# Kernel tuning notes

Hardware: AMD Instinct MI355X
Metric: run time of the kernel (lower is better)

The kernel has to match this reference:

```python
import jax, jax.numpy as jnp
import numpy as np

BS, N, D_N, D_PROJ, ROLE_DIM, K, F, H, L = 4, 1024, 128, 64, 16, 512, 512, 8, 4
HD = F // H
FF = 4 * F
EB_HID = max(H, 8)
TOK_IN = 3 + 3 * D_PROJ + ROLE_DIM + 2  # 213


def _ln(x, g, b, eps=1e-5):
    m = x.mean(-1, keepdims=True)
    v = ((x - m) ** 2).mean(-1, keepdims=True)
    return (x - m) * jax.lax.rsqrt(v + eps) * g + b


def _gelu(x):
    return jax.nn.gelu(x, approximate=False)  # torch nn.GELU default is exact erf


def setup_inputs():
    key = jax.random.key(0)
    ks = jax.random.split(key, 32)
    p = lambda i, shape, s=0.02: jax.random.normal(ks[i], shape, jnp.float32) * s
    return {
        'h': jax.random.normal(ks[0], (BS, N, D_N), jnp.float32),
        'msg': jax.random.normal(ks[1], (BS, N, D_N), jnp.float32),
        'received': jax.random.normal(ks[2], (BS, N, D_N), jnp.float32),
        'W': jax.random.normal(ks[3], (BS, N, N), jnp.float32) * 0.1,
        'hebbian': jax.random.normal(ks[4], (BS, N, N), jnp.float32) * 0.1,
        'decay': jax.random.uniform(ks[5], (BS, N), jnp.float32),
        's_live': jax.random.normal(ks[6], (BS,), jnp.float32),
        's_ema': jax.random.normal(ks[7], (BS,), jnp.float32),
        'role_id': jax.random.randint(ks[8], (N,), 0, 3),
        'Wh': p(9, (D_N, D_PROJ)),
        'Wme': p(10, (D_N, D_PROJ)),
        'Wmr': p(11, (D_N, D_PROJ)),
        'role_emb': p(12, (3, ROLE_DIM)),
        'tok_W1': p(13, (TOK_IN, F)), 'tok_b1': jnp.zeros((F,), jnp.float32),
        'tok_W2': p(14, (F, F)), 'tok_b2': jnp.zeros((F,), jnp.float32),
        'eb_W1': p(15, (3, EB_HID)), 'eb_b1': jnp.zeros((EB_HID,), jnp.float32),
        'eb_W2': p(16, (EB_HID, H)), 'eb_b2': jnp.zeros((H,), jnp.float32),
        'ln1_g': jnp.ones((L, F), jnp.float32), 'ln1_b': jnp.zeros((L, F), jnp.float32),
        'qkv_W': p(17, (L, F, 3 * F)),
        'out_W': p(18, (L, F, F)),
        'ln2_g': jnp.ones((L, F), jnp.float32), 'ln2_b': jnp.zeros((L, F), jnp.float32),
        'ffn_W1': p(19, (L, F, FF)), 'ffn_b1': jnp.zeros((L, FF), jnp.float32),
        'ffn_W2': p(20, (L, FF, F)), 'ffn_b2': jnp.zeros((L, F), jnp.float32),
        'pool_g': jnp.ones((F,), jnp.float32), 'pool_b': jnp.zeros((F,), jnp.float32),
        'head_W': p(21, (F, K)), 'head_b': jnp.zeros((K,), jnp.float32),
    }


def _forward(h, msg, received, W, hebbian, decay, s_live, s_ema, role_id,
             Wh, Wme, Wmr, role_emb, tok_W1, tok_b1, tok_W2, tok_b2,
             eb_W1, eb_b1, eb_W2, eb_b2, ln1_g, ln1_b, qkv_W, out_W,
             ln2_g, ln2_b, ffn_W1, ffn_b1, ffn_W2, ffn_b2,
             pool_g, pool_b, head_W, head_b):
    # ---- build_tokens: [BS,N,F] ----
    h_p = h @ Wh
    me_p = msg @ Wme
    mr_p = received @ Wmr
    h_norm = jnp.linalg.norm(h, axis=-1, keepdims=True)
    msg_norm = jnp.linalg.norm(msg, axis=-1, keepdims=True)
    dec = decay[..., None]
    role_e = jnp.broadcast_to(role_emb[role_id][None], (BS, N, ROLE_DIM))
    sl = jnp.broadcast_to(s_live[:, None, None], (BS, N, 1))
    se = jnp.broadcast_to(s_ema[:, None, None], (BS, N, 1))
    tok_in = jnp.concatenate([h_norm, msg_norm, dec, h_p, me_p, mr_p, role_e, sl, se], axis=-1)
    tokens = _gelu(tok_in @ tok_W1 + tok_b1) @ tok_W2 + tok_b2
    # ---- build_edge_bias: [BS,H,N,N] ----
    asym = W - jnp.swapaxes(W, -1, -2)
    ef = jnp.stack([W, hebbian, asym], axis=-1)           # [BS,N,N,3]
    bias = _gelu(ef @ eb_W1 + eb_b1) @ eb_W2 + eb_b2      # [BS,N,N,H]
    bias = jnp.transpose(bias, (0, 3, 1, 2))              # [BS,H,N,N]
    # ---- attention blocks ----
    scale = 1.0 / np.sqrt(HD).astype(np.float32)
    x = tokens
    for l in range(L):
        hn = _ln(x, ln1_g[l], ln1_b[l])
        qkv = (hn @ qkv_W[l]).reshape(BS, N, 3, H, HD)
        q = jnp.transpose(qkv[:, :, 0], (0, 2, 1, 3))     # [BS,H,N,HD]
        k = jnp.transpose(qkv[:, :, 1], (0, 2, 1, 3))
        v = jnp.transpose(qkv[:, :, 2], (0, 2, 1, 3))
        scores = jnp.einsum('bhnd,bhmd->bhnm', q, k) * scale + bias
        attn = jax.nn.softmax(scores, axis=-1)
        ao = jnp.einsum('bhnm,bhmd->bhnd', attn, v)
        ao = jnp.transpose(ao, (0, 2, 1, 3)).reshape(BS, N, F)
        x = x + ao @ out_W[l]
        hn2 = _ln(x, ln2_g[l], ln2_b[l])
        x = x + _gelu(hn2 @ ffn_W1[l] + ffn_b1[l]) @ ffn_W2[l] + ffn_b2[l]
    pooled = _ln(x, pool_g, pool_b).mean(axis=1)
    logits = pooled @ head_W + head_b
    return logits, x


def reference(h, msg, received, W, hebbian, decay, s_live, s_ema, role_id,
              Wh, Wme, Wmr, role_emb, tok_W1, tok_b1, tok_W2, tok_b2,
              eb_W1, eb_b1, eb_W2, eb_b2, ln1_g, ln1_b, qkv_W, out_W,
              ln2_g, ln2_b, ffn_W1, ffn_b1, ffn_W2, ffn_b2,
              pool_g, pool_b, head_W, head_b):
    return _forward(h, msg, received, W, hebbian, decay, s_live, s_ema, role_id,
                    Wh, Wme, Wmr, role_emb, tok_W1, tok_b1, tok_W2, tok_b2,
                    eb_W1, eb_b1, eb_W2, eb_b2, ln1_g, ln1_b, qkv_W, out_W,
                    ln2_g, ln2_b, ffn_W1, ffn_b1, ffn_W2, ffn_b2,
                    pool_g, pool_b, head_W, head_b)
```

## Files before the change

kernel.cpp:

```cpp
#include <hip/hip_runtime.h>
#include <hip/hip_bf16.h>
#include <math.h>

#define BS 4
#define N_ 1024
#define DN 128
#define DP 64
#define RD 16
#define KOUT 512
#define F_ 512
#define H_ 8
#define HD_ 64
#define L_ 4
#define FFN_ 2048
#define TI 213
#define TIP 256

typedef __attribute__((ext_vector_type(8))) short bf16x8;
typedef __attribute__((ext_vector_type(4))) float f32x4;
typedef unsigned int u32;
typedef unsigned short u16;

union U8 { u32 w[4]; bf16x8 v; };

__device__ __forceinline__ float gelu_fast(float x) {
    float u2 = 1.5957691216f * fmaf(0.044715f * x, x * x, x);
    return x / (1.f + __expf(-u2));
}

__device__ __forceinline__ float gelu_small(float u) {
    float q = u * u;
    float t = fmaf(q, -0.06649038f, 0.39894228f);
    return fmaf(q, t, 0.5f * u);
}

__device__ __forceinline__ void gl_lds16(const void* g, void* l) {
    __builtin_amdgcn_global_load_lds((const __attribute__((address_space(1))) void*)g,
                                     (__attribute__((address_space(3))) void*)l, 16, 0, 0);
}

__device__ __forceinline__ u32 bf16rn(float f) {
    u32 b = __builtin_bit_cast(u32, f);
    return (b + 0x7fffu + ((b >> 16) & 1u)) >> 16;
}
__device__ __forceinline__ float bf2f(u16 u) {
    return __builtin_bit_cast(float, (u32)u << 16);
}

__global__ __launch_bounds__(256) void k_tokin(
    const float* __restrict__ h, const float* __restrict__ msg, const float* __restrict__ rcv,
    const float* __restrict__ decay, const float* __restrict__ s_live, const float* __restrict__ s_ema,
    const int* __restrict__ role_id, const float* __restrict__ role_emb,
    const float* __restrict__ Wh, const float* __restrict__ Wme, const float* __restrict__ Wmr,
    __hip_bfloat16* __restrict__ tok_in)
{
    int row = blockIdx.x;
    int b = row >> 10, n = row & 1023;
    __shared__ float hs[DN], ms[DN], rs[DN];
    __shared__ float proj[192];
    __shared__ float norms[2];
    int tid = threadIdx.x;
    const float* hp = h + (size_t)row * DN;
    const float* mp = msg + (size_t)row * DN;
    const float* rp = rcv + (size_t)row * DN;
    for (int i = tid; i < DN; i += 256) { hs[i] = hp[i]; ms[i] = mp[i]; rs[i] = rp[i]; }
    __syncthreads();
    if (tid < 128) {
        int lane = tid & 63;
        const float* src = (tid < 64) ? hs : ms;
        float v = src[lane]*src[lane] + src[lane+64]*src[lane+64];
        #pragma unroll
        for (int m = 32; m >= 1; m >>= 1) v += __shfl_xor(v, m);
        if (lane == 0) norms[tid >> 6] = sqrtf(v);
    }
    if (tid < 192) {
        int which = tid >> 6, col = tid & 63;
        const float* src = (which == 0) ? hs : ((which == 1) ? ms : rs);
        const float* Wp  = (which == 0) ? Wh : ((which == 1) ? Wme : Wmr);
        float acc = 0.f;
        for (int k2 = 0; k2 < DN; ++k2) acc = fmaf(src[k2], Wp[k2 * DP + col], acc);
        proj[tid] = acc;
    }
    __syncthreads();
    __hip_bfloat16* out = tok_in + (size_t)row * TIP;
    if (tid < TIP) {
        float v = 0.f;
        if (tid == 0) v = norms[0];
        else if (tid == 1) v = norms[1];
        else if (tid == 2) v = decay[b * N_ + n];
        else if (tid < 195) v = proj[tid - 3];
        else if (tid < 211) v = role_emb[role_id[n] * RD + (tid - 195)];
        else if (tid == 211) v = s_live[b];
        else if (tid == 212) v = s_ema[b];
        out[tid] = __float2bfloat16(v);
    }
}

__global__ __launch_bounds__(256) void k_convall(
    const float* __restrict__ qkvW, const float* __restrict__ outW,
    const float* __restrict__ f1W, const float* __restrict__ f2W,
    const float* __restrict__ t1, const float* __restrict__ t2,
    __hip_bfloat16* __restrict__ wq, __hip_bfloat16* __restrict__ wo,
    __hip_bfloat16* __restrict__ w1, __hip_bfloat16* __restrict__ w2,
    __hip_bfloat16* __restrict__ t1w, __hip_bfloat16* __restrict__ t2w)
{
    int tile = blockIdx.x;
    const float* in; __hip_bfloat16* out;
    int K, N, Kpad, r2, nx, ky;
    if (tile < 3072) {
        int z = tile / 768; r2 = tile % 768;
        nx = r2 % 48; ky = r2 / 48;
        in = qkvW + (size_t)z * F_ * 3 * F_; out = wq + (size_t)z * 3 * F_ * F_;
        K = F_; N = 3 * F_; Kpad = F_;
    } else if (tile < 4096) {
        int t = tile - 3072; int z = t / 256; r2 = t % 256;
        nx = r2 % 16; ky = r2 / 16;
        in = outW + (size_t)z * F_ * F_; out = wo + (size_t)z * F_ * F_;
        K = F_; N = F_; Kpad = F_;
    } else if (tile < 8192) {
        int t = tile - 4096; int z = t / 1024; r2 = t % 1024;
        nx = r2 % 64; ky = r2 / 64;
        in = f1W + (size_t)z * F_ * FFN_; out = w1 + (size_t)z * FFN_ * F_;
        K = F_; N = FFN_; Kpad = F_;
    } else if (tile < 12288) {
        int t = tile - 8192; int z = t / 1024; r2 = t % 1024;
        nx = r2 % 16; ky = r2 / 16;
        in = f2W + (size_t)z * FFN_ * F_; out = w2 + (size_t)z * F_ * FFN_;
        K = FFN_; N = F_; Kpad = FFN_;
    } else if (tile < 12416) {
        int t = tile - 12288;
        nx = t % 16; ky = t / 16;
        in = t1; out = t1w; K = TI; N = F_; Kpad = TIP;
    } else {
        int t = tile - 12416;
        nx = t % 16; ky = t / 16;
        in = t2; out = t2w; K = F_; N = F_; Kpad = F_;
    }
    int k0 = ky * 32, n0 = nx * 32;
    __shared__ float tls[32][33];
    int c = threadIdx.x & 31, r = threadIdx.x >> 5;
    #pragma unroll
    for (int i = 0; i < 4; ++i) {
        int rr = r + i*8;
        tls[rr][c] = (k0 + rr < K) ? in[(size_t)(k0 + rr) * N + n0 + c] : 0.f;
    }
    __syncthreads();
    #pragma unroll
    for (int i = 0; i < 4; ++i) {
        int rr = r + i*8;
        out[(size_t)(n0 + rr) * Kpad + k0 + c] = __float2bfloat16(tls[c][rr]);
    }
}

template<int BM, int BN, int EPI, bool OBF>
__global__ __launch_bounds__(256) void k_gemm_bf16(
    const __hip_bfloat16* __restrict__ Ah, int lda,
    const __hip_bfloat16* __restrict__ Bth, int ldb,
    void* __restrict__ Cout, int ldc, int Kc,
    const float* __restrict__ bias,
    const float* __restrict__ resid, int ldres,
    void* __restrict__ aux)
{
    constexpr int MFM = BM / 32;
    constexpr int MFN = BN / 32;
    constexpr int HALF = (BM + BN) * 64;
    constexpr int NLOAD = (BM + BN) / 32;
    constexpr int ACH = BM / 32;
    __shared__ __align__(16) short lds[2 * HALF];
    const short* A  = (const short*)Ah;
    const short* Bt = (const short*)Bth;
    int tid = threadIdx.x, w = tid >> 6, lane = tid & 63;
    int wr = w >> 1, wc = w & 1;
    int m0 = blockIdx.y * BM, n0 = blockIdx.x * BN;

    f32x4 acc[MFM][MFN];
    #pragma unroll
    for (int m = 0; m < MFM; ++m)
        #pragma unroll
        for (int n = 0; n < MFN; ++n)
            acc[m][n] = (f32x4){0.f, 0.f, 0.f, 0.f};

    int ebase = w * 512 + lane * 8;

    auto stage = [&](int buf, int k0) {
        short* L = lds + buf * HALF;
        #pragma unroll
        for (int i = 0; i < NLOAD; ++i) {
            int e = i * 2048 + ebase;
            if (i < ACH) {
                int r = e >> 6, c = e & 63;
                int cs = c ^ (8 * (r & 7));
                gl_lds16(A + (size_t)(m0 + r) * lda + k0 + cs, L + e);
            } else {
                int eb = e - BM * 64;
                int r = eb >> 6, c = eb & 63;
                int cs = c ^ (8 * (r & 7));
                gl_lds16(Bt + (size_t)(n0 + r) * ldb + k0 + cs, L + e);
            }
        }
    };

    int nt = Kc >> 6;
    int buf = 0;
    stage(0, 0);
    __syncthreads();
    int cl = lane & 15, g = lane >> 4;
    for (int t = 0; t < nt; ++t) {
        if (t + 1 < nt) stage(buf ^ 1, (t + 1) << 6);
        const short* La = lds + buf * HALF;
        const short* Lb = La + BM * 64;
        #pragma unroll
        for (int kk = 0; kk < 2; ++kk) {
            bf16x8 av[MFM], bv[MFN];
            #pragma unroll
            for (int m = 0; m < MFM; ++m) {
                int r = wr * (BM/2) + m * 16 + cl;
                av[m] = *(const bf16x8*)&La[r * 64 + ((kk*32 + g*8) ^ (8*(r&7)))];
            }
            #pragma unroll
            for (int n = 0; n < MFN; ++n) {
                int r = wc * (BN/2) + n * 16 + cl;
                bv[n] = *(const bf16x8*)&Lb[r * 64 + ((kk*32 + g*8) ^ (8*(r&7)))];
            }
            #pragma unroll
            for (int m = 0; m < MFM; ++m)
                #pragma unroll
                for (int n = 0; n < MFN; ++n)
                    acc[m][n] = __builtin_amdgcn_mfma_f32_16x16x32_bf16(av[m], bv[n], acc[m][n], 0, 0, 0);
        }
        __syncthreads();
        buf ^= 1;
    }

    int r4 = g * 4;

    if (EPI == 5) {
        __hip_bfloat16* Cb = (__hip_bfloat16*)Cout;
        u16* vtp = (u16*)aux;
        if (n0 >= 1024) {
            int bb = m0 >> 10;
            #pragma unroll
            for (int m = 0; m < MFM; ++m) {
                int grow0 = m0 + wr * (BM/2) + m * 16 + r4;
                int nloc = grow0 & 1023;
                #pragma unroll
                for (int n = 0; n < MFN; ++n) {
                    int rel = n0 - 1024 + wc * (BN / 2) + n * 16 + cl;
                    int hh2 = rel >> 6, d = rel & 63;
                    u32 lo = bf16rn(acc[m][n][0]) | (bf16rn(acc[m][n][1]) << 16);
                    u32 hi = bf16rn(acc[m][n][2]) | (bf16rn(acc[m][n][3]) << 16);
                    uint2 v2 = {lo, hi};
                    *(uint2*)&vtp[((size_t)((bb * 8 + hh2) * 64 + d)) * 1024 + nloc] = v2;
                }
            }
        } else {
            #pragma unroll
            for (int m = 0; m < MFM; ++m) {
                #pragma unroll
                for (int n = 0; n < MFN; ++n) {
                    int gcol = n0 + wc * (BN / 2) + n * 16 + cl;
                    #pragma unroll
                    for (int r = 0; r < 4; ++r) {
                        int grow = m0 + wr * (BM/2) + m * 16 + r4 + r;
                        Cb[(size_t)grow * ldc + gcol] = __float2bfloat16(acc[m][n][r]);
                    }
                }
            }
        }
        return;
    }

    float* Cf = (float*)Cout;
    __hip_bfloat16* Cb = (__hip_bfloat16*)Cout;
    #pragma unroll
    for (int m = 0; m < MFM; ++m) {
        #pragma unroll
        for (int n = 0; n < MFN; ++n) {
            int gcol = n0 + wc * (BN / 2) + n * 16 + cl;
            #pragma unroll
            for (int r = 0; r < 4; ++r) {
                int grow = m0 + wr * (BM/2) + m * 16 + r4 + r;
                float v = acc[m][n][r];
                if (EPI == 1 || EPI == 2 || EPI == 3) v += bias[gcol];
                if (EPI == 2) v = gelu_fast(v);
                if (EPI == 3 || EPI == 4) v += resid[(size_t)grow * ldres + gcol];
                if (OBF) Cb[(size_t)grow * ldc + gcol] = __float2bfloat16(v);
                else     Cf[(size_t)grow * ldc + gcol] = v;
            }
        }
    }
}

__global__ __launch_bounds__(256) void k_ln(const float* __restrict__ x, const float* __restrict__ g,
                                            const float* __restrict__ bb, __hip_bfloat16* __restrict__ out)
{
    int w = threadIdx.x >> 6, lane = threadIdx.x & 63;
    int row = blockIdx.x * 4 + w;
    const float* xr = x + (size_t)row * F_;
    float v[8];
    float s = 0.f;
    #pragma unroll
    for (int i = 0; i < 8; ++i) { v[i] = xr[lane + 64*i]; s += v[i]; }
    #pragma unroll
    for (int m = 32; m >= 1; m >>= 1) s += __shfl_xor(s, m);
    float mean = s * (1.f/512.f);
    float vs = 0.f;
    #pragma unroll
    for (int i = 0; i < 8; ++i) { float d = v[i] - mean; vs = fmaf(d, d, vs); }
    #pragma unroll
    for (int m = 32; m >= 1; m >>= 1) vs += __shfl_xor(vs, m);
    float rstd = rsqrtf(vs * (1.f/512.f) + 1e-5f);
    __hip_bfloat16* orow = out + (size_t)row * F_;
    #pragma unroll
    for (int i = 0; i < 8; ++i) {
        int c = lane + 64*i;
        orow[c] = __float2bfloat16((v[i] - mean) * rstd * g[c] + bb[c]);
    }
}

__global__ __launch_bounds__(256) void k_bias(
    const float* __restrict__ W, const float* __restrict__ Heb,
    const float* __restrict__ eW1, const float* __restrict__ eb1,
    const float* __restrict__ eW2, const float* __restrict__ eb2,
    u16* __restrict__ bias_out)
{
    int b = blockIdx.z;
    int i0 = blockIdx.x * 128, j0 = blockIdx.y * 32;
    __shared__ float Wt[128][33];
    __shared__ float Ht[128][33];
    __shared__ float Wr[32][128];
    const float* Wb = W + (size_t)b * N_ * N_;
    const float* Hb = Heb + (size_t)b * N_ * N_;
    int tid = threadIdx.x;
    {
        int c2 = tid & 31, r = tid >> 5;
        #pragma unroll
        for (int k = 0; k < 16; ++k) {
            int rr = r + k * 8;
            Wt[rr][c2] = Wb[(size_t)(i0 + rr) * N_ + j0 + c2];
            Ht[rr][c2] = Hb[(size_t)(i0 + rr) * N_ + j0 + c2];
        }
        int r2 = tid >> 3, c8 = (tid & 7) * 16;
        #pragma unroll
        for (int k = 0; k < 4; ++k)
            *(float4*)&Wr[r2][c8 + 4*k] = *(const float4*)&Wb[(size_t)(j0 + r2) * N_ + i0 + c8 + 4*k];
    }
    float A[8], Bc[8], Cc[8], Dd[8], W2[8][8], b2v[8];
    #pragma unroll
    for (int k = 0; k < 8; ++k) {
        A[k] = eW1[k]; Bc[k] = eW1[8 + k]; Cc[k] = eW1[16 + k]; Dd[k] = eb1[k];
        b2v[k] = eb2[k];
        #pragma unroll
        for (int hh = 0; hh < 8; ++hh) W2[k][hh] = eW2[k * 8 + hh];
    }
    __syncthreads();
    int c = tid & 31;
    int j8 = tid >> 5;
    #pragma unroll
    for (int pass = 0; pass < 4; ++pass) {
        int jj = j8 + pass * 8;
        float4 wt4 = *(const float4*)&Wr[jj][4 * c];
        float wT[4] = {wt4.x, wt4.y, wt4.z, wt4.w};
        float out[4][8];
        #pragma unroll
        for (int s = 0; s < 4; ++s) {
            float w  = Wt[4*c + s][jj];
            float he = Ht[4*c + s][jj];
            float as = w - wT[s];
            #pragma unroll
            for (int hh = 0; hh < 8; ++hh) out[s][hh] = b2v[hh];
            #pragma unroll
            for (int k = 0; k < 8; ++k) {
                float u = fmaf(w, A[k], fmaf(he, Bc[k], fmaf(as, Cc[k], Dd[k])));
                float hid = gelu_small(u);
                #pragma unroll
                for (int hh = 0; hh < 8; ++hh) out[s][hh] = fmaf(hid, W2[k][hh], out[s][hh]);
            }
        }
        size_t base = ((size_t)(b * H_) * N_ + (j0 + jj)) * N_ + i0 + 4 * c;
        #pragma unroll
        for (int hh = 0; hh < 8; ++hh) {
            u32 lo = bf16rn(out[0][hh]) | (bf16rn(out[1][hh]) << 16);
            u32 hi = bf16rn(out[2][hh]) | (bf16rn(out[3][hh]) << 16);
            uint2 v2 = {lo, hi};
            *(uint2*)&bias_out[base + (size_t)hh * N_ * N_] = v2;
        }
    }
}

__global__ __launch_bounds__(256) void k_attn_mfma(
    const u16* __restrict__ qkvb,
    const u16* __restrict__ vt,
    const u16* __restrict__ biasT,
    u16* __restrict__ ao)
{
    int bh = blockIdx.x, b = bh >> 3, hh = bh & 7;
    int r0 = blockIdx.y * 64;
    int tid = threadIdx.x, w = tid >> 6, lane = tid & 63;
    int cl = lane & 15, g = lane >> 4;
    int q0 = r0 + w * 16;

    __shared__ __align__(16) u16 lds[2 * 12288];

    bf16x8 qreg[2];
    {
        const u16* qrow = qkvb + (size_t)(b*N_ + q0 + cl) * 1536 + hh*64 + g*8;
        qreg[0] = *(const bf16x8*)qrow;
        qreg[1] = *(const bf16x8*)(qrow + 32);
    }
    f32x4 oacc[4];
    #pragma unroll
    for (int db = 0; db < 4; ++db) oacc[db] = (f32x4){0.f, 0.f, 0.f, 0.f};
    float mreg = -1e30f, lreg = 0.f;

    int ebase = w * 512 + lane * 8;
    const u16* bias_base = biasT + (size_t)bh * N_ * N_ + r0;
    auto stage = [&](int bufi, int t) {
        u16* Ld = (u16*)lds + bufi * 12288;
        int c0 = t * 64;
        #pragma unroll
        for (int i = 0; i < 2; ++i) {
            int e = i * 2048 + ebase;
            int n = e >> 6, c = e & 63;
            int cs = c ^ (8 * (n & 7));
            gl_lds16(qkvb + (size_t)(b*N_ + c0 + n)*1536 + 512 + hh*64 + cs,
                     Ld + i*2048 + w*512);
            gl_lds16(vt + (size_t)(bh*64 + n)*1024 + c0 + cs,
                     Ld + 4096 + i*2048 + w*512);
            gl_lds16(bias_base + (size_t)(c0 + n) * N_ + c,
                     Ld + 8192 + i*2048 + w*512);
        }
    };
    stage(0, 0);
    __syncthreads();
    int buf = 0;

    for (int t = 0; t < 16; ++t) {
        if (t < 15) stage(buf ^ 1, t + 1);
        const u16* LK = (const u16*)lds + buf * 12288;
        const u16* LV = LK + 4096;
        const u16* LB = LK + 8192;

        f32x4 sacc[4];
        #pragma unroll
        for (int mf = 0; mf < 4; ++mf) sacc[mf] = (f32x4){0.f, 0.f, 0.f, 0.f};
        __builtin_amdgcn_s_setprio(1);
        #pragma unroll
        for (int kh = 0; kh < 2; ++kh)
            #pragma unroll
            for (int mf = 0; mf < 4; ++mf) {
                int n = mf*16 + cl;
                bf16x8 af = *(const bf16x8*)&LK[n*64 + ((kh*32 + g*8) ^ (8*(n&7)))];
                sacc[mf] = __builtin_amdgcn_mfma_f32_16x16x32_bf16(af, qreg[kh], sacc[mf], 0, 0, 0);
            }
        __builtin_amdgcn_s_setprio(0);

        float p[4][4];
        float mx = -1e30f;
        int qc = w*16 + cl;
        #pragma unroll
        for (int mf = 0; mf < 4; ++mf)
            #pragma unroll
            for (int r = 0; r < 4; ++r) {
                float bv = bf2f(LB[(mf*16 + g*4 + r) * 64 + qc]);
                float s = fmaf(sacc[mf][r], 0.125f, bv);
                p[mf][r] = s;
                mx = fmaxf(mx, s);
            }
        mx = fmaxf(mx, __shfl_xor(mx, 16));
        mx = fmaxf(mx, __shfl_xor(mx, 32));
        float mnew = fmaxf(mreg, mx);
        float corr = __expf(mreg - mnew);
        float rs = 0.f;
        #pragma unroll
        for (int mf = 0; mf < 4; ++mf)
            #pragma unroll
            for (int r = 0; r < 4; ++r) {
                p[mf][r] = __expf(p[mf][r] - mnew);
                rs += p[mf][r];
            }
        rs += __shfl_xor(rs, 16);
        rs += __shfl_xor(rs, 32);
        lreg = lreg * corr + rs;
        mreg = mnew;

        #pragma unroll
        for (int r = 0; r < 4; ++r) {
            float c4 = __shfl(corr, g*4 + r);
            #pragma unroll
            for (int db = 0; db < 4; ++db) oacc[db][r] *= c4;
        }

        u32 u[4][2];
        #pragma unroll
        for (int mf = 0; mf < 4; ++mf) {
            u[mf][0] = bf16rn(p[mf][0]) | (bf16rn(p[mf][1]) << 16);
            u[mf][1] = bf16rn(p[mf][2]) | (bf16rn(p[mf][3]) << 16);
        }
        U8 pa[2];
        #pragma unroll
        for (int kh = 0; kh < 2; ++kh)
            #pragma unroll
            for (int wd = 0; wd < 4; ++wd) {
                int src = 16 * (2*(g&1) + (wd>>1)) + cl;
                u32 va = (u32)__shfl((int)u[2*kh][wd&1], src);
                u32 vb = (u32)__shfl((int)u[2*kh+1][wd&1], src);
                pa[kh].w[wd] = (g >> 1) ? vb : va;
            }

        __builtin_amdgcn_s_setprio(1);
        #pragma unroll
        for (int kh = 0; kh < 2; ++kh)
            #pragma unroll
            for (int db = 0; db < 4; ++db) {
                int d = db*16 + cl;
                bf16x8 vf = *(const bf16x8*)&LV[d*64 + ((kh*32 + g*8) ^ (8*(d&7)))];
                oacc[db] = __builtin_amdgcn_mfma_f32_16x16x32_bf16(pa[kh].v, vf, oacc[db], 0, 0, 0);
            }
        __builtin_amdgcn_s_setprio(0);
        __syncthreads();
        buf ^= 1;
    }

    float inv = 1.f / lreg;
    #pragma unroll
    for (int r = 0; r < 4; ++r) {
        float iv = __shfl(inv, g*4 + r);
        int q = q0 + g*4 + r;
        #pragma unroll
        for (int db = 0; db < 4; ++db)
            ao[(size_t)(b*N_ + q)*F_ + hh*64 + db*16 + cl] = (u16)bf16rn(oacc[db][r] * iv);
    }
}

__global__ __launch_bounds__(256) void k_poolp(const float* __restrict__ x, float* __restrict__ partial)
{
    int chunk = blockIdx.x, b = blockIdx.y;
    int w = threadIdx.x >> 6, lane = threadIdx.x & 63;
    float acc[8] = {0.f,0.f,0.f,0.f,0.f,0.f,0.f,0.f};
    #pragma unroll
    for (int rr = 0; rr < 4; ++rr) {
        int row = b * N_ + chunk * 16 + w * 4 + rr;
        const float* xr = x + (size_t)row * F_;
        float v[8];
        float s = 0.f;
        #pragma unroll
        for (int i = 0; i < 8; ++i) { v[i] = xr[lane + 64*i]; s += v[i]; }
        #pragma unroll
        for (int m = 32; m >= 1; m >>= 1) s += __shfl_xor(s, m);
        float mean = s * (1.f/512.f);
        float vs = 0.f;
        #pragma unroll
        for (int i = 0; i < 8; ++i) { float d = v[i] - mean; vs = fmaf(d, d, vs); }
        #pragma unroll
        for (int m = 32; m >= 1; m >>= 1) vs += __shfl_xor(vs, m);
        float rstd = rsqrtf(vs * (1.f/512.f) + 1e-5f);
        #pragma unroll
        for (int i = 0; i < 8; ++i) acc[i] += (v[i] - mean) * rstd;
    }
    __shared__ float red[4][512];
    #pragma unroll
    for (int i = 0; i < 8; ++i) red[w][lane + 64*i] = acc[i];
    __syncthreads();
    #pragma unroll
    for (int k = 0; k < 2; ++k) {
        int f = threadIdx.x * 2 + k;
        float s = red[0][f] + red[1][f] + red[2][f] + red[3][f];
        partial[((size_t)b * 64 + chunk) * 512 + f] = s;
    }
}

__global__ __launch_bounds__(256) void k_head2(const float* __restrict__ partial,
    const float* __restrict__ g, const float* __restrict__ bb,
    const float* __restrict__ hW, const float* __restrict__ hb, float* __restrict__ logits)
{
    int b = blockIdx.y;
    int tid = threadIdx.x;
    __shared__ float pooled[512];
    __shared__ float red[256];
    #pragma unroll
    for (int k = 0; k < 2; ++k) {
        int f = tid * 2 + k;
        float s = 0.f;
        const float* pp = partial + (size_t)b * 64 * 512 + f;
        #pragma unroll 8
        for (int c = 0; c < 64; ++c) s += pp[c * 512];
        pooled[f] = s * (1.f/1024.f) * g[f] + bb[f];
    }
    __syncthreads();
    int k0 = blockIdx.x * 64 + (tid & 63);
    int fq = tid >> 6;
    float s = 0.f;
    #pragma unroll 4
    for (int f = fq * 128; f < fq * 128 + 128; ++f)
        s = fmaf(pooled[f], hW[(size_t)f * KOUT + k0], s);
    red[tid] = s;
    __syncthreads();
    if (fq == 0) {
        s = red[tid] + red[tid + 64] + red[tid + 128] + red[tid + 192];
        logits[b * KOUT + k0] = s + hb[k0];
    }
}

extern "C" void kernel_launch(void* const* d_in, const int* in_sizes, int n_in,
                              void* d_out, int out_size, void* d_ws, size_t ws_size,
                              hipStream_t stream)
{
    (void)in_sizes; (void)n_in; (void)out_size; (void)ws_size;
    const float* h      = (const float*)d_in[0];
    const float* msg    = (const float*)d_in[1];
    const float* rcv    = (const float*)d_in[2];
    const float* W      = (const float*)d_in[3];
    const float* heb    = (const float*)d_in[4];
    const float* decay  = (const float*)d_in[5];
    const float* s_live = (const float*)d_in[6];
    const float* s_ema  = (const float*)d_in[7];
    const int*   role   = (const int*)d_in[8];
    const float* Wh     = (const float*)d_in[9];
    const float* Wme    = (const float*)d_in[10];
    const float* Wmr    = (const float*)d_in[11];
    const float* role_emb = (const float*)d_in[12];
    const float* tok_W1 = (const float*)d_in[13];
    const float* tok_b1 = (const float*)d_in[14];
    const float* tok_W2 = (const float*)d_in[15];
    const float* tok_b2 = (const float*)d_in[16];
    const float* eW1    = (const float*)d_in[17];
    const float* eb1    = (const float*)d_in[18];
    const float* eW2    = (const float*)d_in[19];
    const float* eb2    = (const float*)d_in[20];
    const float* ln1_g  = (const float*)d_in[21];
    const float* ln1_b  = (const float*)d_in[22];
    const float* qkv_W  = (const float*)d_in[23];
    const float* out_W  = (const float*)d_in[24];
    const float* ln2_g  = (const float*)d_in[25];
    const float* ln2_b  = (const float*)d_in[26];
    const float* ffn_W1 = (const float*)d_in[27];
    const float* ffn_b1 = (const float*)d_in[28];
    const float* ffn_W2 = (const float*)d_in[29];
    const float* ffn_b2 = (const float*)d_in[30];
    const float* pool_g = (const float*)d_in[31];
    const float* pool_b = (const float*)d_in[32];
    const float* head_W = (const float*)d_in[33];
    const float* head_b = (const float*)d_in[34];

    float* logits = (float*)d_out;
    float* x = logits + BS * KOUT;

    char* ws = (char*)d_ws;
    size_t o = 0;
    auto alloc = [&](size_t bytes) { char* p = ws + o; o += (bytes + 255) & ~255ul; return p; };

    __hip_bfloat16* tok_in = (__hip_bfloat16*)alloc((size_t)BS * N_ * TIP * 2);
    char* scratch          = alloc((size_t)BS * N_ * 3 * F_ * 4);
    __hip_bfloat16* hn     = (__hip_bfloat16*)alloc((size_t)BS * N_ * F_ * 2);
    __hip_bfloat16* aob    = (__hip_bfloat16*)alloc((size_t)BS * N_ * F_ * 2);
    u16* vtb               = (u16*)alloc((size_t)BS * H_ * HD_ * N_ * 2);
    float* partial         = (float*)alloc((size_t)BS * 64 * 512 * 4);
    __hip_bfloat16* wq     = (__hip_bfloat16*)alloc((size_t)L_ * 3 * F_ * F_ * 2);
    __hip_bfloat16* wo     = (__hip_bfloat16*)alloc((size_t)L_ * F_ * F_ * 2);
    __hip_bfloat16* w1     = (__hip_bfloat16*)alloc((size_t)L_ * FFN_ * F_ * 2);
    __hip_bfloat16* w2     = (__hip_bfloat16*)alloc((size_t)L_ * F_ * FFN_ * 2);
    __hip_bfloat16* t1w    = (__hip_bfloat16*)alloc((size_t)F_ * TIP * 2);
    __hip_bfloat16* t2w    = (__hip_bfloat16*)alloc((size_t)F_ * F_ * 2);
    u16* biasT             = (u16*)alloc((size_t)BS * H_ * N_ * N_ * 2);

    u16* qkvb = (u16*)scratch;
    __hip_bfloat16* midb = (__hip_bfloat16*)scratch;
    __hip_bfloat16* tokmid = (__hip_bfloat16*)scratch;

    const int M = BS * N_;

    k_convall<<<dim3(12672), 256, 0, stream>>>(qkv_W, out_W, ffn_W1, ffn_W2, tok_W1, tok_W2,
                                               wq, wo, w1, w2, t1w, t2w);

    k_tokin<<<dim3(M), 256, 0, stream>>>(h, msg, rcv, decay, s_live, s_ema, role, role_emb,
                                         Wh, Wme, Wmr, tok_in);
    k_bias<<<dim3(N_/128, N_/32, BS), 256, 0, stream>>>(W, heb, eW1, eb1, eW2, eb2, biasT);

    k_gemm_bf16<64, 64, 2, true><<<dim3(F_/64, M/64), 256, 0, stream>>>(
        tok_in, TIP, t1w, TIP, tokmid, F_, TIP, tok_b1, nullptr, 0, nullptr);
    k_gemm_bf16<64, 64, 1, false><<<dim3(F_/64, M/64), 256, 0, stream>>>(
        tokmid, F_, t2w, F_, x, F_, F_, tok_b2, nullptr, 0, nullptr);

    for (int l = 0; l < L_; ++l) {
        k_ln<<<dim3(M/4), 256, 0, stream>>>(x, ln1_g + l*F_, ln1_b + l*F_, hn);
        k_gemm_bf16<128, 64, 5, true><<<dim3(3*F_/64, M/128), 256, 0, stream>>>(
            hn, F_, wq + (size_t)l*3*F_*F_, F_, qkvb, 3*F_, F_, nullptr, nullptr, 0, vtb);
        k_attn_mfma<<<dim3(BS*H_, N_/64), 256, 0, stream>>>(qkvb, vtb, biasT, (u16*)aob);
        k_gemm_bf16<64, 64, 4, false><<<dim3(F_/64, M/64), 256, 0, stream>>>(
            aob, F_, wo + (size_t)l*F_*F_, F_, x, F_, F_, nullptr, x, F_, nullptr);
        k_ln<<<dim3(M/4), 256, 0, stream>>>(x, ln2_g + l*F_, ln2_b + l*F_, hn);
        k_gemm_bf16<128, 128, 2, true><<<dim3(FFN_/128, M/128), 256, 0, stream>>>(
            hn, F_, w1 + (size_t)l*FFN_*F_, F_, midb, FFN_, F_, ffn_b1 + l*FFN_, nullptr, 0, nullptr);
        k_gemm_bf16<64, 64, 3, false><<<dim3(F_/64, M/64), 256, 0, stream>>>(
            midb, FFN_, w2 + (size_t)l*F_*FFN_, FFN_, x, F_, FFN_, ffn_b2 + l*F_, x, F_, nullptr);
    }

    k_poolp<<<dim3(64, BS), 256, 0, stream>>>(x, partial);
    k_head2<<<dim3(KOUT/64, BS), 256, 0, stream>>>(partial, pool_g, pool_b, head_W, head_b, logits);
}
```

Measured before the change: 490.9 us.

## Store residual stream in bf16 and use lazy softmax rescaling in attention

The residual activation x is now kept in bf16 across all layers instead of fp32. GEMM epilogues read and write the bf16 residual, and layernorm and pooling load vectorized bf16x8. Pooling writes the final fp32 x to the output. Separately, the flash-attention loop only rescales the running max and output accumulators when the new max exceeds the old one by more than 8. This trades residual precision and accumulated rounding error for lower memory traffic and less per-tile exp and multiply work.

```diff
diff --git a/kernel.cpp b/kernel.cpp
--- a/kernel.cpp
+++ b/kernel.cpp
@@ -158,7 +158,7 @@
     const __hip_bfloat16* __restrict__ Bth, int ldb,
     void* __restrict__ Cout, int ldc, int Kc,
     const float* __restrict__ bias,
-    const float* __restrict__ resid, int ldres,
+    const void* __restrict__ resid, int ldres,
     void* __restrict__ aux)
 {
     constexpr int MFM = BM / 32;
@@ -272,6 +272,7 @@
 
     float* Cf = (float*)Cout;
     __hip_bfloat16* Cb = (__hip_bfloat16*)Cout;
+    const u16* residb = (const u16*)resid;
     #pragma unroll
     for (int m = 0; m < MFM; ++m) {
         #pragma unroll
@@ -283,7 +284,7 @@
                 float v = acc[m][n][r];
                 if (EPI == 1 || EPI == 2 || EPI == 3) v += bias[gcol];
                 if (EPI == 2) v = gelu_fast(v);
-                if (EPI == 3 || EPI == 4) v += resid[(size_t)grow * ldres + gcol];
+                if (EPI == 3 || EPI == 4) v += bf2f(residb[(size_t)grow * ldres + gcol]);
                 if (OBF) Cb[(size_t)grow * ldc + gcol] = __float2bfloat16(v);
                 else     Cf[(size_t)grow * ldc + gcol] = v;
             }
@@ -291,16 +292,17 @@
     }
 }
 
-__global__ __launch_bounds__(256) void k_ln(const float* __restrict__ x, const float* __restrict__ g,
-                                            const float* __restrict__ bb, __hip_bfloat16* __restrict__ out)
+__global__ __launch_bounds__(256) void k_ln(const u16* __restrict__ xb, const float* __restrict__ g,
+                                            const float* __restrict__ bb, u16* __restrict__ out)
 {
     int w = threadIdx.x >> 6, lane = threadIdx.x & 63;
     int row = blockIdx.x * 4 + w;
-    const float* xr = x + (size_t)row * F_;
+    const u16* xr = xb + (size_t)row * F_;
+    bf16x8 raw = *(const bf16x8*)&xr[lane * 8];
     float v[8];
     float s = 0.f;
     #pragma unroll
-    for (int i = 0; i < 8; ++i) { v[i] = xr[lane + 64*i]; s += v[i]; }
+    for (int i = 0; i < 8; ++i) { v[i] = bf2f((u16)raw[i]); s += v[i]; }
     #pragma unroll
     for (int m = 32; m >= 1; m >>= 1) s += __shfl_xor(s, m);
     float mean = s * (1.f/512.f);
@@ -310,12 +312,16 @@
     #pragma unroll
     for (int m = 32; m >= 1; m >>= 1) vs += __shfl_xor(vs, m);
     float rstd = rsqrtf(vs * (1.f/512.f) + 1e-5f);
-    __hip_bfloat16* orow = out + (size_t)row * F_;
-    #pragma unroll
-    for (int i = 0; i < 8; ++i) {
-        int c = lane + 64*i;
-        orow[c] = __float2bfloat16((v[i] - mean) * rstd * g[c] + bb[c]);
-    }
+    int c0 = lane * 8;
+    u32 w4[4];
+    #pragma unroll
+    for (int i = 0; i < 4; ++i) {
+        float o0 = (v[2*i]   - mean) * rstd * g[c0 + 2*i]   + bb[c0 + 2*i];
+        float o1 = (v[2*i+1] - mean) * rstd * g[c0 + 2*i+1] + bb[c0 + 2*i+1];
+        w4[i] = bf16rn(o0) | (bf16rn(o1) << 16);
+    }
+    uint4 pack = {w4[0], w4[1], w4[2], w4[3]};
+    *(uint4*)&out[(size_t)row * F_ + c0] = pack;
 }
 
 __global__ __launch_bounds__(256) void k_bias(
@@ -469,27 +475,29 @@
             }
         mx = fmaxf(mx, __shfl_xor(mx, 16));
         mx = fmaxf(mx, __shfl_xor(mx, 32));
-        float mnew = fmaxf(mreg, mx);
-        float corr = __expf(mreg - mnew);
+        if (__any(mx > mreg + 8.f)) {
+            float mnew = fmaxf(mreg, mx);
+            float corr = __expf(mreg - mnew);
+            lreg *= corr;
+            mreg = mnew;
+            #pragma unroll
+            for (int r = 0; r < 4; ++r) {
+                float c4 = __shfl(corr, g*4 + r);
+                #pragma unroll
+                for (int db = 0; db < 4; ++db) oacc[db][r] *= c4;
+            }
+        }
         float rs = 0.f;
         #pragma unroll
         for (int mf = 0; mf < 4; ++mf)
             #pragma unroll
             for (int r = 0; r < 4; ++r) {
-                p[mf][r] = __expf(p[mf][r] - mnew);
+                p[mf][r] = __expf(p[mf][r] - mreg);
                 rs += p[mf][r];
             }
         rs += __shfl_xor(rs, 16);
         rs += __shfl_xor(rs, 32);
-        lreg = lreg * corr + rs;
-        mreg = mnew;
-
-        #pragma unroll
-        for (int r = 0; r < 4; ++r) {
-            float c4 = __shfl(corr, g*4 + r);
-            #pragma unroll
-            for (int db = 0; db < 4; ++db) oacc[db][r] *= c4;
-        }
+        lreg += rs;
 
         u32 u[4][2];
         #pragma unroll
@@ -533,7 +541,8 @@
     }
 }
 
-__global__ __launch_bounds__(256) void k_poolp(const float* __restrict__ x, float* __restrict__ partial)
+__global__ __launch_bounds__(256) void k_poolp(const u16* __restrict__ xb, float* __restrict__ xout,
+                                               float* __restrict__ partial)
 {
     int chunk = blockIdx.x, b = blockIdx.y;
     int w = threadIdx.x >> 6, lane = threadIdx.x & 63;
@@ -541,11 +550,17 @@
     #pragma unroll
     for (int rr = 0; rr < 4; ++rr) {
         int row = b * N_ + chunk * 16 + w * 4 + rr;
-        const float* xr = x + (size_t)row * F_;
+        const u16* xr = xb + (size_t)row * F_;
+        bf16x8 raw = *(const bf16x8*)&xr[lane * 8];
         float v[8];
         float s = 0.f;
         #pragma unroll
-        for (int i = 0; i < 8; ++i) { v[i] = xr[lane + 64*i]; s += v[i]; }
+        for (int i = 0; i < 8; ++i) { v[i] = bf2f((u16)raw[i]); s += v[i]; }
+        float* xo = xout + (size_t)row * F_ + lane * 8;
+        float4 o0 = {v[0], v[1], v[2], v[3]};
+        float4 o1 = {v[4], v[5], v[6], v[7]};
+        *(float4*)xo = o0;
+        *(float4*)(xo + 4) = o1;
         #pragma unroll
         for (int m = 32; m >= 1; m >>= 1) s += __shfl_xor(s, m);
         float mean = s * (1.f/512.f);
@@ -560,7 +575,7 @@
     }
     __shared__ float red[4][512];
     #pragma unroll
-    for (int i = 0; i < 8; ++i) red[w][lane + 64*i] = acc[i];
+    for (int i = 0; i < 8; ++i) red[w][lane * 8 + i] = acc[i];
     __syncthreads();
     #pragma unroll
     for (int k = 0; k < 2; ++k) {
@@ -644,7 +659,7 @@
     const float* head_b = (const float*)d_in[34];
 
     float* logits = (float*)d_out;
-    float* x = logits + BS * KOUT;
+    float* xout = logits + BS * KOUT;
 
     char* ws = (char*)d_ws;
     size_t o = 0;
@@ -652,6 +667,7 @@
 
     __hip_bfloat16* tok_in = (__hip_bfloat16*)alloc((size_t)BS * N_ * TIP * 2);
     char* scratch          = alloc((size_t)BS * N_ * 3 * F_ * 4);
+    u16* xb                = (u16*)alloc((size_t)BS * N_ * F_ * 2);
     __hip_bfloat16* hn     = (__hip_bfloat16*)alloc((size_t)BS * N_ * F_ * 2);
     __hip_bfloat16* aob    = (__hip_bfloat16*)alloc((size_t)BS * N_ * F_ * 2);
     u16* vtb               = (u16*)alloc((size_t)BS * H_ * HD_ * N_ * 2);
@@ -679,23 +695,23 @@
 
     k_gemm_bf16<64, 64, 2, true><<<dim3(F_/64, M/64), 256, 0, stream>>>(
         tok_in, TIP, t1w, TIP, tokmid, F_, TIP, tok_b1, nullptr, 0, nullptr);
-    k_gemm_bf16<64, 64, 1, false><<<dim3(F_/64, M/64), 256, 0, stream>>>(
-        tokmid, F_, t2w, F_, x, F_, F_, tok_b2, nullptr, 0, nullptr);
+    k_gemm_bf16<64, 64, 1, true><<<dim3(F_/64, M/64), 256, 0, stream>>>(
+        tokmid, F_, t2w, F_, xb, F_, F_, tok_b2, nullptr, 0, nullptr);
 
     for (int l = 0; l < L_; ++l) {
-        k_ln<<<dim3(M/4), 256, 0, stream>>>(x, ln1_g + l*F_, ln1_b + l*F_, hn);
+        k_ln<<<dim3(M/4), 256, 0, stream>>>(xb, ln1_g + l*F_, ln1_b + l*F_, (u16*)hn);
         k_gemm_bf16<128, 64, 5, true><<<dim3(3*F_/64, M/128), 256, 0, stream>>>(
             hn, F_, wq + (size_t)l*3*F_*F_, F_, qkvb, 3*F_, F_, nullptr, nullptr, 0, vtb);
         k_attn_mfma<<<dim3(BS*H_, N_/64), 256, 0, stream>>>(qkvb, vtb, biasT, (u16*)aob);
-        k_gemm_bf16<64, 64, 4, false><<<dim3(F_/64, M/64), 256, 0, stream>>>(
-            aob, F_, wo + (size_t)l*F_*F_, F_, x, F_, F_, nullptr, x, F_, nullptr);
-        k_ln<<<dim3(M/4), 256, 0, stream>>>(x, ln2_g + l*F_, ln2_b + l*F_, hn);
+        k_gemm_bf16<64, 64, 4, true><<<dim3(F_/64, M/64), 256, 0, stream>>>(
+            aob, F_, wo + (size_t)l*F_*F_, F_, xb, F_, F_, nullptr, xb, F_, nullptr);
+        k_ln<<<dim3(M/4), 256, 0, stream>>>(xb, ln2_g + l*F_, ln2_b + l*F_, (u16*)hn);
         k_gemm_bf16<128, 128, 2, true><<<dim3(FFN_/128, M/128), 256, 0, stream>>>(
             hn, F_, w1 + (size_t)l*FFN_*F_, F_, midb, FFN_, F_, ffn_b1 + l*FFN_, nullptr, 0, nullptr);
-        k_gemm_bf16<64, 64, 3, false><<<dim3(F_/64, M/64), 256, 0, stream>>>(
-            midb, FFN_, w2 + (size_t)l*F_*FFN_, FFN_, x, F_, FFN_, ffn_b2 + l*F_, x, F_, nullptr);
-    }
-
-    k_poolp<<<dim3(64, BS), 256, 0, stream>>>(x, partial);
+        k_gemm_bf16<64, 64, 3, true><<<dim3(F_/64, M/64), 256, 0, stream>>>(
+            midb, FFN_, w2 + (size_t)l*F_*FFN_, FFN_, xb, F_, FFN_, ffn_b2 + l*F_, xb, F_, nullptr);
+    }
+
+    k_poolp<<<dim3(64, BS), 256, 0, stream>>>(xb, xout, partial);
     k_head2<<<dim3(KOUT/64, BS), 256, 0, stream>>>(partial, pool_g, pool_b, head_W, head_b, logits);
 }
```

Result: faster. 470.0 us (-4.2%).
